# Kernel optimization log

Hardware: AMD Instinct MI355X
Metric: run time of the kernel (lower is better)

Reference implementation:

```python
import jax, jax.numpy as jnp
import numpy as np

HEADS, LEVELS, POINTS, ZANCH = 8, 4, 8, 4
EMBED = 256
SHAPES = np.array([[92, 160], [46, 80], [23, 40], [12, 20]], dtype=np.int32)


def setup_inputs() -> dict:
    key = jax.random.key(0)
    k = jax.random.split(key, 9)
    bs, nq = 1, 10000
    nv = int((SHAPES[:, 0].astype(np.int64) * SHAPES[:, 1]).sum())  # 19560
    f32 = jnp.float32
    return dict(
        query=jax.random.normal(k[0], (bs, nq, EMBED), f32),
        value=jax.random.normal(k[1], (bs, nv, EMBED), f32),
        query_pos=0.1 * jax.random.normal(k[2], (bs, nq, EMBED), f32),
        reference_points=jax.random.uniform(k[3], (bs, nq, ZANCH, 2), dtype=f32),
        spatial_shapes=jnp.asarray(SHAPES),
        W_off=0.01 * jax.random.normal(k[4], (EMBED, HEADS * LEVELS * POINTS * 2), f32),
        b_off=0.5 * jax.random.normal(k[5], (HEADS * LEVELS * POINTS * 2,), f32),
        W_attn=0.01 * jax.random.normal(k[6], (EMBED, HEADS * LEVELS * POINTS), f32),
        b_attn=jnp.zeros((HEADS * LEVELS * POINTS,), f32),
        W_val=(1.0 / np.sqrt(EMBED)) * jax.random.normal(k[7], (EMBED, EMBED), f32),
        b_val=jnp.zeros((EMBED,), f32),
        W_out=(1.0 / np.sqrt(EMBED)) * jax.random.normal(k[8], (EMBED, EMBED), f32),
        b_out=jnp.zeros((EMBED,), f32),
    )


def _bilinear(v_l, x, y, Hl, Wl):
    # v_l: [bs, heads, Hl*Wl, d]; x, y: [bs, nq, heads, P] pixel coords
    # (torch grid_sample, align_corners=False, zero padding): px = loc*W - 0.5
    bs, nq, heads, P = x.shape
    d = v_l.shape[-1]
    x0 = jnp.floor(x)
    y0 = jnp.floor(y)
    lx = x - x0
    ly = y - y0
    x0i = x0.astype(jnp.int32)
    y0i = y0.astype(jnp.int32)

    def corner(xi, yi, w):
        valid = (xi >= 0) & (xi < Wl) & (yi >= 0) & (yi < Hl)
        idx = jnp.clip(yi, 0, Hl - 1) * Wl + jnp.clip(xi, 0, Wl - 1)
        idxr = idx.transpose(0, 2, 1, 3).reshape(bs, heads, nq * P)
        g = jnp.take_along_axis(v_l, idxr[..., None], axis=2)  # [bs,heads,nq*P,d]
        g = g.reshape(bs, heads, nq, P, d).transpose(0, 2, 1, 3, 4)
        return g * (w * valid.astype(w.dtype))[..., None]

    return (corner(x0i, y0i, (1 - lx) * (1 - ly))
            + corner(x0i + 1, y0i, lx * (1 - ly))
            + corner(x0i, y0i + 1, (1 - lx) * ly)
            + corner(x0i + 1, y0i + 1, lx * ly))


def reference(query, value, query_pos, reference_points, spatial_shapes,
              W_off, b_off, W_attn, b_attn, W_val, b_val, W_out, b_out):
    shapes = np.asarray(spatial_shapes)  # static per-level (H, W)
    bs, nq, E = query.shape
    heads = HEADS
    L = shapes.shape[0]
    P = W_off.shape[1] // (heads * L * 2)
    Z = reference_points.shape[2]
    d = E // heads

    residual = query
    q = query + query_pos
    v = (value @ W_val + b_val).reshape(bs, -1, heads, d)

    off = (q @ W_off + b_off).reshape(bs, nq, heads, L, P, 2)
    attn = jax.nn.softmax((q @ W_attn + b_attn).reshape(bs, nq, heads, L * P), axis=-1)
    attn = attn.reshape(bs, nq, heads, L, P)

    # normalize offsets by (W, H) per level, add Z-anchor reference points
    norm = jnp.asarray(np.stack([shapes[:, 1], shapes[:, 0]], -1), off.dtype)  # [L,2]
    off = off / norm[None, None, None, :, None, :]
    loc = (reference_points[:, :, None, None, None, :, :]
           + off.reshape(bs, nq, heads, L, P // Z, Z, 2)).reshape(bs, nq, heads, L, P, 2)

    starts = np.concatenate([[0], np.cumsum(shapes[:, 0].astype(np.int64) * shapes[:, 1])])
    out = jnp.zeros((bs, nq, heads, d), q.dtype)
    for l in range(L):  # small fixed loop over pyramid levels
        Hl, Wl = int(shapes[l, 0]), int(shapes[l, 1])
        v_l = v[:, int(starts[l]):int(starts[l + 1])].transpose(0, 2, 1, 3)  # [bs,heads,HW,d]
        x = loc[:, :, :, l, :, 0] * Wl - 0.5
        y = loc[:, :, :, l, :, 1] * Hl - 0.5
        sampled = _bilinear(v_l, x, y, Hl, Wl)  # [bs,nq,heads,P,d]
        out = out + (sampled * attn[:, :, :, l, :, None]).sum(axis=3)

    out = out.reshape(bs, nq, E) @ W_out + b_out
    return out + residual  # dropout is identity at eval
```

## Files before the change

### kernel.cpp

```cpp
#include <hip/hip_runtime.h>
#include <hip/hip_bf16.h>
#include <math.h>

typedef __hip_bfloat16 bf16;
typedef short short8_t __attribute__((ext_vector_type(8)));
typedef float f32x4 __attribute__((ext_vector_type(4)));

#define EMBED 256
#define ZANCH 4

__global__ __launch_bounds__(256) void k_prep(
    const float* __restrict__ Woff, const float* __restrict__ Wattn,
    const float* __restrict__ Wval, const float* __restrict__ Wout,
    bf16* __restrict__ wt,
    const float* __restrict__ value, bf16* __restrict__ vb,
    const float* __restrict__ query, const float* __restrict__ query_pos,
    bf16* __restrict__ qb)
{
    const int b = blockIdx.x;
    const int tid = threadIdx.x;
    if (b < 320) {
        __shared__ float tile[32][33];
        const int tn = b >> 3, tk = b & 7;
        const int r = tid >> 5, c = tid & 31;
        const int n0 = tn * 32, k0t = tk * 32;
#pragma unroll
        for (int rr = r; rr < 32; rr += 8) {
            const int k = k0t + rr;
            const int n = n0 + c;
            float val;
            if (n < 512)       val = Woff[(size_t)k * 512 + n];
            else if (n < 768)  val = Wattn[(size_t)k * 256 + (n - 512)];
            else if (n < 1024) val = Wval[(size_t)k * 256 + (n - 768)];
            else               val = Wout[(size_t)k * 256 + (n - 1024)];
            tile[rr][c] = val;
        }
        __syncthreads();
#pragma unroll
        for (int rr = r; rr < 32; rr += 8) {
            const int n = n0 + rr;
            const int k = k0t + c;
            wt[(size_t)n * 256 + k] = __float2bfloat16(tile[c][rr]);
        }
    } else if (b < 5210) {
        size_t i = ((size_t)(b - 320) * 256 + tid) * 4;
        float4 a = *(const float4*)(value + i);
        vb[i + 0] = __float2bfloat16(a.x);
        vb[i + 1] = __float2bfloat16(a.y);
        vb[i + 2] = __float2bfloat16(a.z);
        vb[i + 3] = __float2bfloat16(a.w);
    } else {
        size_t i = ((size_t)(b - 5210) * 256 + tid) * 4;
        float4 a = *(const float4*)(query + i);
        float4 p = *(const float4*)(query_pos + i);
        qb[i + 0] = __float2bfloat16(a.x + p.x);
        qb[i + 1] = __float2bfloat16(a.y + p.y);
        qb[i + 2] = __float2bfloat16(a.z + p.z);
        qb[i + 3] = __float2bfloat16(a.w + p.w);
    }
}

__device__ __forceinline__ void mfma_core_64x256(
    const bf16* __restrict__ A, const bf16* __restrict__ Bt,
    int M, int row0, int nwave, f32x4 acc[4][4])
{
    const int lane = threadIdx.x & 63;
    const int c16 = lane & 15, quad = lane >> 4;
    size_t aoff[4], boff[4];
#pragma unroll
    for (int mt = 0; mt < 4; ++mt) {
        int r = row0 + mt * 16 + c16;
        r = (r < M) ? r : (M - 1);
        aoff[mt] = (size_t)r * 256 + quad * 8;
    }
#pragma unroll
    for (int nt = 0; nt < 4; ++nt)
        boff[nt] = (size_t)(nwave + nt * 16 + c16) * 256 + quad * 8;

#pragma unroll
    for (int k0 = 0; k0 < 256; k0 += 32) {
        short8_t a[4], b[4];
#pragma unroll
        for (int mt = 0; mt < 4; ++mt) a[mt] = *(const short8_t*)(A + aoff[mt] + k0);
#pragma unroll
        for (int nt = 0; nt < 4; ++nt) b[nt] = *(const short8_t*)(Bt + boff[nt] + k0);
#pragma unroll
        for (int mt = 0; mt < 4; ++mt)
#pragma unroll
            for (int nt = 0; nt < 4; ++nt)
                acc[mt][nt] = __builtin_amdgcn_mfma_f32_16x16x32_bf16(
                    a[mt], b[nt], acc[mt][nt], 0, 0, 0);
    }
}

__global__ __launch_bounds__(256) void k_gemm_vp(
    bf16* __restrict__ vb, const bf16* __restrict__ Btv,
    const float* __restrict__ bv, int Mv,
    const bf16* __restrict__ qb, const bf16* __restrict__ Btcat,
    const float* __restrict__ boff, const float* __restrict__ battn,
    float* __restrict__ raw, int Mq)
{
    const int lane = threadIdx.x & 63;
    const int c16 = lane & 15, quad = lane >> 4;
    const int nwave = (threadIdx.x >> 6) * 64;

    if (blockIdx.y == 3) {
        if ((int)blockIdx.x >= (Mv + 63) / 64) return;
        const int row0 = blockIdx.x * 64;
        f32x4 acc[4][4] = {};
        mfma_core_64x256(vb, Btv, Mv, row0, nwave, acc);
#pragma unroll
        for (int nt = 0; nt < 4; ++nt) {
            int colg = nwave + nt * 16 + c16;
            float bias = bv[colg];
#pragma unroll
            for (int mt = 0; mt < 4; ++mt)
#pragma unroll
                for (int reg = 0; reg < 4; ++reg) {
                    int row = row0 + mt * 16 + quad * 4 + reg;
                    if (row < Mv)
                        vb[(size_t)row * 256 + colg] = __float2bfloat16(acc[mt][nt][reg] + bias);
                }
        }
    } else {
        if ((int)blockIdx.x >= (Mq + 63) / 64) return;
        const int row0 = blockIdx.x * 64;
        const int n0slab = blockIdx.y * 256;
        f32x4 acc[4][4] = {};
        mfma_core_64x256(qb, Btcat + (size_t)n0slab * 256, Mq, row0, nwave, acc);
#pragma unroll
        for (int nt = 0; nt < 4; ++nt) {
            int colg = n0slab + nwave + nt * 16 + c16;
            float bias = (colg < 512) ? boff[colg] : battn[colg - 512];
#pragma unroll
            for (int mt = 0; mt < 4; ++mt)
#pragma unroll
                for (int reg = 0; reg < 4; ++reg) {
                    int row = row0 + mt * 16 + quad * 4 + reg;
                    if (row < Mq)
                        raw[(size_t)row * 768 + colg] = acc[mt][nt][reg] + bias;
                }
        }
    }
}

__global__ __launch_bounds__(256) void k_sample(
    const bf16* __restrict__ v, const float* __restrict__ raw,
    const float* __restrict__ refpts, bf16* __restrict__ outa, int nq)
{
    __shared__ int2 lds_pair[2][1024];
    const int tid = threadIdx.x;
    const int q0 = blockIdx.x * 2;

    {
        const int l = (tid >> 3) & 3;
        const int p = tid & 7;
        const int z = p & (ZANCH - 1);
        const float Wlf = (l == 0) ? 160.f : (l == 1) ? 80.f : (l == 2) ? 40.f : 20.f;
        const float Hlf = (l == 0) ? 92.f : (l == 1) ? 46.f : (l == 2) ? 23.f : 12.f;
        const int Wli = (l == 0) ? 160 : (l == 1) ? 80 : (l == 2) ? 40 : 20;
        const int Hli = (l == 0) ? 92 : (l == 1) ? 46 : (l == 2) ? 23 : 12;
        const int Stl = (l == 0) ? 0 : (l == 1) ? 14720 : (l == 2) ? 18400 : 19320;

#pragma unroll
        for (int r = 0; r < 2; ++r) {
            const int q = q0 + r;
            const float ox = raw[(size_t)q * 768 + 2 * tid];
            const float oy = raw[(size_t)q * 768 + 2 * tid + 1];
            const float lg = raw[(size_t)q * 768 + 512 + tid];

            float m = lg;
            for (int o = 16; o > 0; o >>= 1) m = fmaxf(m, __shfl_xor(m, o, 32));
            float e = __expf(lg - m);
            float s = e;
            for (int o = 16; o > 0; o >>= 1) s += __shfl_xor(s, o, 32);
            const float aw = e / s;

            const float refx = refpts[(size_t)q * 8 + z * 2 + 0];
            const float refy = refpts[(size_t)q * 8 + z * 2 + 1];
            const float px = refx * Wlf + ox - 0.5f;
            const float py = refy * Hlf + oy - 0.5f;

            const float x0f = floorf(px), y0f = floorf(py);
            const int x0 = (int)x0f, y0 = (int)y0f;
            const float lx = px - x0f, ly = py - y0f;
            const float cw[4] = { (1.f - lx) * (1.f - ly), lx * (1.f - ly),
                                  (1.f - lx) * ly,         lx * ly };
#pragma unroll
            for (int c = 0; c < 4; ++c) {
                const int xi = x0 + (c & 1);
                const int yi = y0 + (c >> 1);
                const bool valid = (xi >= 0) && (xi < Wli) && (yi >= 0) && (yi < Hli);
                const int xc = min(max(xi, 0), Wli - 1);
                const int yc = min(max(yi, 0), Hli - 1);
                const float w = valid ? (cw[c] * aw) : 0.f;
                lds_pair[r][tid * 4 + c] = make_int2(Stl + yc * Wli + xc, __float_as_int(w));
            }
        }
    }
    __syncthreads();

    const int qsel = tid >> 7;
    const int slot = tid & 127;
    const int h = slot >> 4;
    const int cp = slot & 15;
    const int col = h * 32 + cp * 2;
    const int ebase = h * 128;
    const bf16* vcol = v + col;

    float acc0 = 0.f, acc1 = 0.f;
#pragma unroll 2
    for (int bb = 0; bb < 128; bb += 16) {
        int2 pr[16];
#pragma unroll
        for (int i = 0; i < 16; ++i) pr[i] = lds_pair[qsel][ebase + bb + i];
        int dv[16];
#pragma unroll
        for (int i = 0; i < 16; ++i)
            dv[i] = *(const int*)(vcol + (size_t)pr[i].x * 256);
#pragma unroll
        for (int i = 0; i < 16; ++i) {
            const float w = __int_as_float(pr[i].y);
            acc0 = fmaf(w, __int_as_float(dv[i] << 16), acc0);
            acc1 = fmaf(w, __int_as_float(dv[i] & 0xFFFF0000), acc1);
        }
    }
    __hip_bfloat162 o2;
    o2.x = __float2bfloat16(acc0);
    o2.y = __float2bfloat16(acc1);
    *(__hip_bfloat162*)(outa + (size_t)(q0 + qsel) * 256 + col) = o2;
}

__global__ __launch_bounds__(256) void k_gemm_out(
    const bf16* __restrict__ outa, const bf16* __restrict__ Bto,
    const float* __restrict__ bo, const float* __restrict__ query,
    float* __restrict__ out, int M)
{
    const int row0 = blockIdx.x * 64;
    const int nwave = (threadIdx.x >> 6) * 64;
    f32x4 acc[4][4] = {};
    mfma_core_64x256(outa, Bto, M, row0, nwave, acc);
    const int lane = threadIdx.x & 63;
    const int c16 = lane & 15, quad = lane >> 4;
#pragma unroll
    for (int nt = 0; nt < 4; ++nt) {
        int colg = nwave + nt * 16 + c16;
        float bias = bo[colg];
#pragma unroll
        for (int mt = 0; mt < 4; ++mt)
#pragma unroll
            for (int reg = 0; reg < 4; ++reg) {
                int row = row0 + mt * 16 + quad * 4 + reg;
                if (row < M) {
                    size_t o_ = (size_t)row * 256 + colg;
                    float fv = acc[mt][nt][reg] + bias + query[o_];
                    if (!(fv == fv) || fabsf(fv) > 1e30f) fv = 0.f;
                    out[o_] = fv;
                }
            }
    }
}

extern "C" void kernel_launch(void* const* d_in, const int* in_sizes, int n_in,
                              void* d_out, int out_size, void* d_ws, size_t ws_size,
                              hipStream_t stream)
{
    const float* query     = (const float*)d_in[0];
    const float* value     = (const float*)d_in[1];
    const float* query_pos = (const float*)d_in[2];
    const float* refpts    = (const float*)d_in[3];
    const float* Woff  = (const float*)d_in[5];
    const float* boff  = (const float*)d_in[6];
    const float* Wattn = (const float*)d_in[7];
    const float* battn = (const float*)d_in[8];
    const float* Wval  = (const float*)d_in[9];
    const float* bval  = (const float*)d_in[10];
    const float* Wout  = (const float*)d_in[11];
    const float* bout  = (const float*)d_in[12];
    float* out = (float*)d_out;

    const int nq = in_sizes[0] / EMBED;
    const int nv = in_sizes[1] / EMBED;

    char* base = (char*)d_ws;
    bf16*  wt   = (bf16*)base;
    bf16*  qb   = (bf16*)(base + 655360);
    bf16*  vb   = (bf16*)(base + 5775360);
    float* raw  = (float*)(base + 15790080);
    bf16*  outa = (bf16*)(base + 46510080);
    const bf16* Btcat = wt;
    const bf16* Btv   = wt + 768 * 256;
    const bf16* Bto   = wt + 1024 * 256;

    k_prep<<<7710, 256, 0, stream>>>(Woff, Wattn, Wval, Wout, wt,
                                     value, vb, query, query_pos, qb);
    k_gemm_vp<<<dim3(306, 4), 256, 0, stream>>>(vb, Btv, bval, nv,
                                                qb, Btcat, boff, battn, raw, nq);
    k_sample<<<nq / 2, 256, 0, stream>>>(vb, raw, refpts, outa, nq);
    k_gemm_out<<<(nq + 63) / 64, 256, 0, stream>>>(outa, Bto, bout, query, out, nq);
}
```

Measured before the change: 224.6 us.

## Store projected values head-major and halve GEMM row tiles

The value projection now writes its output in a head-major layout [head][nv][32], so each head's gathered rows sit contiguously and the sampling kernel reads from a compact per-head slab. The sampling LDS tables are split into separate index and weight arrays arranged by corner. All three GEMMs drop from 64-row to 32-row tiles to launch more blocks. The trade-off is an extra workspace buffer, scattered 2-byte stores in the value GEMM epilogue, and less operand reuse per GEMM block.

```diff
diff --git a/kernel.cpp b/kernel.cpp
--- a/kernel.cpp
+++ b/kernel.cpp
@@ -60,15 +60,16 @@
     }
 }
 
-__device__ __forceinline__ void mfma_core_64x256(
+template <int MT>
+__device__ __forceinline__ void mfma_core(
     const bf16* __restrict__ A, const bf16* __restrict__ Bt,
-    int M, int row0, int nwave, f32x4 acc[4][4])
+    int M, int row0, int nwave, f32x4 acc[MT][4])
 {
     const int lane = threadIdx.x & 63;
     const int c16 = lane & 15, quad = lane >> 4;
-    size_t aoff[4], boff[4];
-#pragma unroll
-    for (int mt = 0; mt < 4; ++mt) {
+    size_t aoff[MT], boff[4];
+#pragma unroll
+    for (int mt = 0; mt < MT; ++mt) {
         int r = row0 + mt * 16 + c16;
         r = (r < M) ? r : (M - 1);
         aoff[mt] = (size_t)r * 256 + quad * 8;
@@ -79,13 +80,13 @@
 
 #pragma unroll
     for (int k0 = 0; k0 < 256; k0 += 32) {
-        short8_t a[4], b[4];
-#pragma unroll
-        for (int mt = 0; mt < 4; ++mt) a[mt] = *(const short8_t*)(A + aoff[mt] + k0);
+        short8_t a[MT], b[4];
+#pragma unroll
+        for (int mt = 0; mt < MT; ++mt) a[mt] = *(const short8_t*)(A + aoff[mt] + k0);
 #pragma unroll
         for (int nt = 0; nt < 4; ++nt) b[nt] = *(const short8_t*)(Bt + boff[nt] + k0);
 #pragma unroll
-        for (int mt = 0; mt < 4; ++mt)
+        for (int mt = 0; mt < MT; ++mt)
 #pragma unroll
             for (int nt = 0; nt < 4; ++nt)
                 acc[mt][nt] = __builtin_amdgcn_mfma_f32_16x16x32_bf16(
@@ -94,8 +95,8 @@
 }
 
 __global__ __launch_bounds__(256) void k_gemm_vp(
-    bf16* __restrict__ vb, const bf16* __restrict__ Btv,
-    const float* __restrict__ bv, int Mv,
+    const bf16* __restrict__ vb, const bf16* __restrict__ Btv,
+    const float* __restrict__ bv, bf16* __restrict__ vhl, int Mv,
     const bf16* __restrict__ qb, const bf16* __restrict__ Btcat,
     const float* __restrict__ boff, const float* __restrict__ battn,
     float* __restrict__ raw, int Mq)
@@ -105,35 +106,37 @@
     const int nwave = (threadIdx.x >> 6) * 64;
 
     if (blockIdx.y == 3) {
-        if ((int)blockIdx.x >= (Mv + 63) / 64) return;
-        const int row0 = blockIdx.x * 64;
-        f32x4 acc[4][4] = {};
-        mfma_core_64x256(vb, Btv, Mv, row0, nwave, acc);
+        if ((int)blockIdx.x >= (Mv + 31) / 32) return;
+        const int row0 = blockIdx.x * 32;
+        f32x4 acc[2][4] = {};
+        mfma_core<2>(vb, Btv, Mv, row0, nwave, acc);
 #pragma unroll
         for (int nt = 0; nt < 4; ++nt) {
             int colg = nwave + nt * 16 + c16;
             float bias = bv[colg];
-#pragma unroll
-            for (int mt = 0; mt < 4; ++mt)
+            const int hh = colg >> 5, ch = colg & 31;
+            bf16* vout = vhl + (size_t)hh * Mv * 32 + ch;
+#pragma unroll
+            for (int mt = 0; mt < 2; ++mt)
 #pragma unroll
                 for (int reg = 0; reg < 4; ++reg) {
                     int row = row0 + mt * 16 + quad * 4 + reg;
                     if (row < Mv)
-                        vb[(size_t)row * 256 + colg] = __float2bfloat16(acc[mt][nt][reg] + bias);
+                        vout[(size_t)row * 32] = __float2bfloat16(acc[mt][nt][reg] + bias);
                 }
         }
     } else {
-        if ((int)blockIdx.x >= (Mq + 63) / 64) return;
-        const int row0 = blockIdx.x * 64;
+        if ((int)blockIdx.x >= (Mq + 31) / 32) return;
+        const int row0 = blockIdx.x * 32;
         const int n0slab = blockIdx.y * 256;
-        f32x4 acc[4][4] = {};
-        mfma_core_64x256(qb, Btcat + (size_t)n0slab * 256, Mq, row0, nwave, acc);
+        f32x4 acc[2][4] = {};
+        mfma_core<2>(qb, Btcat + (size_t)n0slab * 256, Mq, row0, nwave, acc);
 #pragma unroll
         for (int nt = 0; nt < 4; ++nt) {
             int colg = n0slab + nwave + nt * 16 + c16;
             float bias = (colg < 512) ? boff[colg] : battn[colg - 512];
 #pragma unroll
-            for (int mt = 0; mt < 4; ++mt)
+            for (int mt = 0; mt < 2; ++mt)
 #pragma unroll
                 for (int reg = 0; reg < 4; ++reg) {
                     int row = row0 + mt * 16 + quad * 4 + reg;
@@ -145,10 +148,11 @@
 }
 
 __global__ __launch_bounds__(256) void k_sample(
-    const bf16* __restrict__ v, const float* __restrict__ raw,
-    const float* __restrict__ refpts, bf16* __restrict__ outa, int nq)
-{
-    __shared__ int2 lds_pair[2][1024];
+    const bf16* __restrict__ vhl, const float* __restrict__ raw,
+    const float* __restrict__ refpts, bf16* __restrict__ outa, int nq, int nv)
+{
+    __shared__ int   sidx[2][4][256];
+    __shared__ float swt[2][4][256];
     const int tid = threadIdx.x;
     const int q0 = blockIdx.x * 2;
 
@@ -193,8 +197,8 @@
                 const bool valid = (xi >= 0) && (xi < Wli) && (yi >= 0) && (yi < Hli);
                 const int xc = min(max(xi, 0), Wli - 1);
                 const int yc = min(max(yi, 0), Hli - 1);
-                const float w = valid ? (cw[c] * aw) : 0.f;
-                lds_pair[r][tid * 4 + c] = make_int2(Stl + yc * Wli + xc, __float_as_int(w));
+                sidx[r][c][tid] = Stl + yc * Wli + xc;
+                swt[r][c][tid]  = valid ? (cw[c] * aw) : 0.f;
             }
         }
     }
@@ -204,31 +208,35 @@
     const int slot = tid & 127;
     const int h = slot >> 4;
     const int cp = slot & 15;
-    const int col = h * 32 + cp * 2;
-    const int ebase = h * 128;
-    const bf16* vcol = v + col;
+    const int e0 = h * 32;
+    const bf16* vbase = vhl + (size_t)h * nv * 32 + cp * 2;
 
     float acc0 = 0.f, acc1 = 0.f;
 #pragma unroll 2
     for (int bb = 0; bb < 128; bb += 16) {
-        int2 pr[16];
-#pragma unroll
-        for (int i = 0; i < 16; ++i) pr[i] = lds_pair[qsel][ebase + bb + i];
+        int   ix[16];
+        float wv[16];
+#pragma unroll
+        for (int j = 0; j < 16; ++j) {
+            const int i = bb + j;
+            const int c = i & 3, lp = i >> 2;
+            ix[j] = sidx[qsel][c][e0 + lp];
+            wv[j] = swt[qsel][c][e0 + lp];
+        }
         int dv[16];
 #pragma unroll
-        for (int i = 0; i < 16; ++i)
-            dv[i] = *(const int*)(vcol + (size_t)pr[i].x * 256);
-#pragma unroll
-        for (int i = 0; i < 16; ++i) {
-            const float w = __int_as_float(pr[i].y);
-            acc0 = fmaf(w, __int_as_float(dv[i] << 16), acc0);
-            acc1 = fmaf(w, __int_as_float(dv[i] & 0xFFFF0000), acc1);
+        for (int j = 0; j < 16; ++j)
+            dv[j] = *(const int*)(vbase + (size_t)ix[j] * 32);
+#pragma unroll
+        for (int j = 0; j < 16; ++j) {
+            acc0 = fmaf(wv[j], __int_as_float(dv[j] << 16), acc0);
+            acc1 = fmaf(wv[j], __int_as_float(dv[j] & 0xFFFF0000), acc1);
         }
     }
     __hip_bfloat162 o2;
     o2.x = __float2bfloat16(acc0);
     o2.y = __float2bfloat16(acc1);
-    *(__hip_bfloat162*)(outa + (size_t)(q0 + qsel) * 256 + col) = o2;
+    *(__hip_bfloat162*)(outa + (size_t)(q0 + qsel) * 256 + h * 32 + cp * 2) = o2;
 }
 
 __global__ __launch_bounds__(256) void k_gemm_out(
@@ -236,10 +244,10 @@
     const float* __restrict__ bo, const float* __restrict__ query,
     float* __restrict__ out, int M)
 {
-    const int row0 = blockIdx.x * 64;
+    const int row0 = blockIdx.x * 32;
     const int nwave = (threadIdx.x >> 6) * 64;
-    f32x4 acc[4][4] = {};
-    mfma_core_64x256(outa, Bto, M, row0, nwave, acc);
+    f32x4 acc[2][4] = {};
+    mfma_core<2>(outa, Bto, M, row0, nwave, acc);
     const int lane = threadIdx.x & 63;
     const int c16 = lane & 15, quad = lane >> 4;
 #pragma unroll
@@ -247,7 +255,7 @@
         int colg = nwave + nt * 16 + c16;
         float bias = bo[colg];
 #pragma unroll
-        for (int mt = 0; mt < 4; ++mt)
+        for (int mt = 0; mt < 2; ++mt)
 #pragma unroll
             for (int reg = 0; reg < 4; ++reg) {
                 int row = row0 + mt * 16 + quad * 4 + reg;
@@ -288,14 +296,15 @@
     bf16*  vb   = (bf16*)(base + 5775360);
     float* raw  = (float*)(base + 15790080);
     bf16*  outa = (bf16*)(base + 46510080);
+    bf16*  vhl  = (bf16*)(base + 51630080);
     const bf16* Btcat = wt;
     const bf16* Btv   = wt + 768 * 256;
     const bf16* Bto   = wt + 1024 * 256;
 
     k_prep<<<7710, 256, 0, stream>>>(Woff, Wattn, Wval, Wout, wt,
                                      value, vb, query, query_pos, qb);
-    k_gemm_vp<<<dim3(306, 4), 256, 0, stream>>>(vb, Btv, bval, nv,
-                                                qb, Btcat, boff, battn, raw, nq);
-    k_sample<<<nq / 2, 256, 0, stream>>>(vb, raw, refpts, outa, nq);
-    k_gemm_out<<<(nq + 63) / 64, 256, 0, stream>>>(outa, Bto, bout, query, out, nq);
-}
+    k_gemm_vp<<<dim3((nv + 31) / 32, 4), 256, 0, stream>>>(vb, Btv, bval, vhl, nv,
+                                                           qb, Btcat, boff, battn, raw, nq);
+    k_sample<<<nq / 2, 256, 0, stream>>>(vhl, raw, refpts, outa, nq, nv);
+    k_gemm_out<<<(nq + 31) / 32, 256, 0, stream>>>(outa, Bto, bout, query, out, nq);
+}
```

Result: no change. 224.3 us (-0.1%).
